# Optimization experiments

Measured on AMD Instinct MI355X. Metric: run time of the kernel, lower is better.

The kernel has to match this reference:

```python
import jax, jax.numpy as jnp
import numpy as np

B, L, H, NH, DH = 2, 4096, 768, 12, 64
W_ = 128          # one-sided sliding window
NL = 2            # encoder layers
VOCAB, OUT, FF = 50265, 384, 3072
EPS = 1e-5


def _ln(x, s, b):
    m = jnp.mean(x, axis=-1, keepdims=True)
    v = jnp.mean((x - m) ** 2, axis=-1, keepdims=True)
    return (x - m) / jnp.sqrt(v + EPS) * s + b


def _attn(x, amask, Wq, bq, Wk, bk, Wv, bv, Wo, bo):
    # x: [B,L,H]; sliding-window attention (one-sided W_) + global token 0
    def heads(Wt, bt):
        return (x @ Wt + bt).reshape(B, L, NH, DH).transpose(0, 2, 1, 3)  # [B,NH,L,DH]
    q, k, v = heads(Wq, bq), heads(Wk, bk), heads(Wv, bv)
    scale = 1.0 / np.sqrt(DH).astype(np.float32)
    C = W_
    nC = L // C
    qc = q.reshape(B, NH, nC, C, DH)

    def blocks(t):  # gather [prev, self, next] key chunks -> [B,NH,nC,3C,DH]
        tc = t.reshape(B, NH, nC, C, DH)
        tp = jnp.pad(tc, ((0, 0), (0, 0), (1, 1), (0, 0), (0, 0)))
        return jnp.concatenate([tp[:, :, :-2], tp[:, :, 1:-1], tp[:, :, 2:]], axis=3)

    k3, v3 = blocks(k), blocks(v)
    s_loc = jnp.einsum('bhncd,bhnkd->bhnck', qc, k3) * scale  # [B,NH,nC,C,3C]

    pos_k = (jnp.arange(nC)[:, None] - 1) * C + jnp.arange(3 * C)[None, :]  # [nC,3C]
    pos_q = jnp.arange(nC)[:, None] * C + jnp.arange(C)[None, :]            # [nC,C]
    within = jnp.abs(pos_q[:, :, None] - pos_k[:, None, :]) <= W_           # [nC,C,3C]
    valid = (pos_k >= 0) & (pos_k < L) & (pos_k != 0)  # key 0 handled as global column
    mk = amask[:, jnp.clip(pos_k, 0, L - 1)] > 0        # [B,nC,3C]
    m = within[None, None] & valid[None, None, :, None, :] & mk[:, None, :, None, :]
    s_loc = jnp.where(m, s_loc, -1e9)

    # every token also attends to the global token 0
    s_g = jnp.einsum('bhld,bhd->bhl', q, k[:, :, 0]) * scale  # [B,NH,L]
    s = jnp.concatenate([s_loc.reshape(B, NH, L, 3 * C), s_g[..., None]], axis=-1)
    p = jax.nn.softmax(s, axis=-1)
    p_loc = p[..., :3 * C].reshape(B, NH, nC, C, 3 * C)
    out = jnp.einsum('bhnck,bhnkd->bhncd', p_loc, v3).reshape(B, NH, L, DH)
    out = out + p[..., -1:] * v[:, :, 0][:, :, None, :]

    # global token 0 attends to everything
    s0 = jnp.einsum('bhd,bhld->bhl', q[:, :, 0], k) * scale
    s0 = jnp.where(amask[:, None, :] > 0, s0, -1e9)
    o0 = jnp.einsum('bhl,bhld->bhd', jax.nn.softmax(s0, axis=-1), v)
    out = out.at[:, :, 0, :].set(o0)

    out = out.transpose(0, 2, 1, 3).reshape(B, L, H)
    return out @ Wo + bo


def setup_inputs() -> dict:
    key = jax.random.key(0)
    ks = jax.random.split(key, 16)
    p = lambda k_, sh: 0.02 * jax.random.normal(k_, sh, jnp.float32)
    return {
        'input_ids': jax.random.randint(ks[0], (B, L), 0, VOCAB, dtype=jnp.int32),
        'attention_mask': jnp.ones((B, L), jnp.int32),
        'word_emb': p(ks[1], (VOCAB, H)),
        'pos_emb': p(ks[2], (L, H)),
        'emb_ln_s': jnp.ones((H,), jnp.float32), 'emb_ln_b': jnp.zeros((H,), jnp.float32),
        'Wq': p(ks[3], (NL, H, H)), 'bq': jnp.zeros((NL, H), jnp.float32),
        'Wk': p(ks[4], (NL, H, H)), 'bk': jnp.zeros((NL, H), jnp.float32),
        'Wv': p(ks[5], (NL, H, H)), 'bv': jnp.zeros((NL, H), jnp.float32),
        'Wo': p(ks[6], (NL, H, H)), 'bo': jnp.zeros((NL, H), jnp.float32),
        'ln1_s': jnp.ones((NL, H), jnp.float32), 'ln1_b': jnp.zeros((NL, H), jnp.float32),
        'W1': p(ks[7], (NL, H, FF)), 'b1': jnp.zeros((NL, FF), jnp.float32),
        'W2': p(ks[8], (NL, FF, H)), 'b2': jnp.zeros((NL, H), jnp.float32),
        'ln2_s': jnp.ones((NL, H), jnp.float32), 'ln2_b': jnp.zeros((NL, H), jnp.float32),
        'Wfc': p(ks[9], (H, OUT)), 'bfc': jnp.zeros((OUT,), jnp.float32),
    }


def reference(input_ids, attention_mask, word_emb, pos_emb, emb_ln_s, emb_ln_b,
              Wq, bq, Wk, bk, Wv, bv, Wo, bo, ln1_s, ln1_b,
              W1, b1, W2, b2, ln2_s, ln2_b, Wfc, bfc):
    x = word_emb[input_ids] + pos_emb[None]
    x = _ln(x, emb_ln_s, emb_ln_b)
    for l in range(NL):
        a = _attn(x, attention_mask, Wq[l], bq[l], Wk[l], bk[l], Wv[l], bv[l], Wo[l], bo[l])
        x = _ln(x + a, ln1_s[l], ln1_b[l])
        h = jax.nn.gelu(x @ W1[l] + b1[l])
        x = _ln(x + h @ W2[l] + b2[l], ln2_s[l], ln2_b[l])
    v_dn = x @ Wfc + bfc           # [B,L,OUT]
    cls = v_dn[:, 0]               # fc(last_hidden[:,0]) == v_dn[:,0]
    return v_dn, cls
```

## Files before the change

### kernel.cpp

```cpp
#include <hip/hip_runtime.h>
#include <hip/hip_bf16.h>
#include <stdint.h>

#define L_SEQ 4096
#define H_DIM 768
#define N_HEADS 12
#define D_HEAD 64
#define N_CHUNK 32
#define CHUNK 128
#define FF_DIM 3072
#define OUT_DIM 384
#define BATCH 2
#define EPS_LN 1e-5f
#define M_ROWS (BATCH * L_SEQ)
#define QKV_LD (3 * H_DIM)
#define NSEG 16

typedef unsigned short u16;
typedef __bf16 bx8 __attribute__((ext_vector_type(8)));
typedef float fx4 __attribute__((ext_vector_type(4)));
typedef u16 ux8 __attribute__((ext_vector_type(8)));

__device__ __forceinline__ u16 f2bf(float f) {
  union { float f; unsigned u; } x; x.f = f;
  unsigned r = x.u + 0x7fffu + ((x.u >> 16) & 1u);
  return (u16)(r >> 16);
}
__device__ __forceinline__ float bf2f(u16 v) {
  union { unsigned u; float f; } x; x.u = ((unsigned)v) << 16;
  return x.f;
}

__device__ __forceinline__ void gload16(const void* g, void* l) {
  __builtin_amdgcn_global_load_lds((const __attribute__((address_space(1))) void*)g,
                                   (__attribute__((address_space(3))) void*)l, 16, 0, 0);
}

template<int OUT_BF16, int DO_GELU, int DO_CLS>
__global__ __launch_bounds__(256, 3)
void gemm_s(const u16* __restrict__ A, const u16* __restrict__ Bt,
            const float* __restrict__ bias,
            float* __restrict__ Cf, u16* __restrict__ Cb,
            float* __restrict__ cls,
            int N, int K)
{
  __shared__ __align__(16) u16 As[128 * 64];
  __shared__ __align__(16) u16 Bs[128 * 64];
  const int tid = threadIdx.x;
  const int lane = tid & 63, w = tid >> 6;
  const int c16 = lane & 15, g = lane >> 4;
  const int wr = w >> 1, wc = w & 1;

  const int nbn = N >> 7;
  int id = blockIdx.x;
  id = (id & 7) * (gridDim.x >> 3) + (id >> 3);
  const int bm = id / nbn, bn = id % nbn;

  const int srow = w * 8 + (lane >> 3);
  const int schunk = (lane & 7) ^ (lane >> 3);
  const u16* sA = A + (size_t)(bm * 128 + srow) * K + schunk * 8;
  const u16* sB = Bt + (size_t)(bn * 128 + srow) * K + schunk * 8;
  const int wdst = w * 512;

  fx4 acc[4][4] = {};

  for (int k0 = 0; k0 < K; k0 += 64) {
    #pragma unroll
    for (int i = 0; i < 4; i++) {
      gload16(sA + (size_t)(i * 32) * K + k0, &As[i * 2048 + wdst]);
      gload16(sB + (size_t)(i * 32) * K + k0, &Bs[i * 2048 + wdst]);
    }
    __syncthreads();
    #pragma unroll
    for (int h = 0; h < 2; h++) {
      bx8 af[4], bf[4];
      #pragma unroll
      for (int m = 0; m < 4; m++) {
        const int row = wr * 64 + m * 16 + c16;
        af[m] = *(const bx8*)&As[row * 64 + (((h << 2) + g) ^ (c16 & 7)) * 8];
      }
      #pragma unroll
      for (int n = 0; n < 4; n++) {
        const int row = wc * 64 + n * 16 + c16;
        bf[n] = *(const bx8*)&Bs[row * 64 + (((h << 2) + g) ^ (c16 & 7)) * 8];
      }
      #pragma unroll
      for (int m = 0; m < 4; m++)
        #pragma unroll
        for (int n = 0; n < 4; n++)
          acc[m][n] = __builtin_amdgcn_mfma_f32_16x16x32_bf16(af[m], bf[n], acc[m][n], 0, 0, 0);
    }
    __syncthreads();
  }

  const int row0 = bm * 128 + wr * 64 + g * 4;
  const int col0 = bn * 128 + wc * 64 + c16;
  #pragma unroll
  for (int n = 0; n < 4; n++) {
    const int col = col0 + n * 16;
    const float bb = bias[col];
    #pragma unroll
    for (int m = 0; m < 4; m++) {
      #pragma unroll
      for (int r = 0; r < 4; r++) {
        float y = acc[m][n][r] + bb;
        if (DO_GELU) {
          const float tt = y;
          y = 0.5f * tt * (1.0f + tanhf(0.7978845608f * (tt + 0.044715f * tt * tt * tt)));
        }
        const int row = row0 + m * 16 + r;
        const size_t idx = (size_t)row * N + col;
        if (OUT_BF16) Cb[idx] = f2bf(y);
        else Cf[idx] = y;
        if (DO_CLS) {
          if ((row & (L_SEQ - 1)) == 0)
            cls[(row >> 12) * OUT_DIM + col] = y;
        }
      }
    }
  }
}

#define KV_W 384
#define P_STR 128

__global__ __launch_bounds__(512, 4)
void attn_local_kernel(const u16* __restrict__ qkv, const int* __restrict__ amask,
                       u16* __restrict__ attnout)
{
  __shared__ __align__(16) u16 Vlds[64 * KV_W];
  __shared__ __align__(16) u16 Plds[8 * 16 * P_STR];

  const int tid = threadIdx.x;
  const int lane = tid & 63, w = tid >> 6;
  const int c16 = lane & 15, g = lane >> 4;

  const int bh = blockIdx.x >> 5;
  const int n = blockIdx.x & 31;
  const int b = bh / N_HEADS, h = bh % N_HEADS;

  const u16* qkvb = qkv + (size_t)b * L_SEQ * QKV_LD + h * D_HEAD;
  const int chunk_lo = n * CHUNK - CHUNK;

  {
    const int d = lane;
    #pragma unroll
    for (int it = 0; it < 6; it++) {
      const int kb = it * 8 + w;
      ux8 vals;
      #pragma unroll
      for (int j = 0; j < 8; j++) {
        int pos = chunk_lo + kb * 8 + j;
        if (pos < 0) pos = 0;
        if (pos >= L_SEQ) pos = L_SEQ - 1;
        vals[j] = qkvb[(size_t)pos * QKV_LD + 2 * H_DIM + d];
      }
      *(ux8*)&Vlds[d * KV_W + ((kb ^ (d & 7)) << 3)] = vals;
    }
  }

  const int qrow = n * CHUNK + w * 16 + c16;
  const u16* qp = qkvb + (size_t)qrow * QKV_LD + g * 8;
  const bx8 aq0 = *(const bx8*)qp;
  const bx8 aq1 = *(const bx8*)(qp + 32);

  unsigned kvm = 0;
  #pragma unroll
  for (int kf = 0; kf < 24; kf++) {
    const int pos = chunk_lo + kf * 16 + c16;
    bool ok = (pos >= 1) && (pos < L_SEQ);
    if (ok) ok = (amask[b * L_SEQ + pos] > 0);
    kvm |= ((unsigned)ok) << kf;
  }

  fx4 s[25];
  #pragma unroll
  for (int kf = 0; kf < 25; kf++) {
    int pos = (kf == 24) ? 0 : chunk_lo + kf * 16 + c16;
    if (pos < 0 || pos >= L_SEQ) pos = 0;
    const u16* kp = qkvb + (size_t)pos * QKV_LD + H_DIM + g * 8;
    const bx8 b0 = *(const bx8*)kp;
    const bx8 b1 = *(const bx8*)(kp + 32);
    fx4 a = {};
    a = __builtin_amdgcn_mfma_f32_16x16x32_bf16(aq0, b0, a, 0, 0, 0);
    a = __builtin_amdgcn_mfma_f32_16x16x32_bf16(aq1, b1, a, 0, 0, 0);
    s[kf] = a;
  }

  const int cq = w * 16 + g * 4;
  float mx[4], sm[4];
  #pragma unroll
  for (int r = 0; r < 4; r++) mx[r] = -3.0e38f;
  #pragma unroll
  for (int kf = 0; kf < 25; kf++) {
    const int j = kf * 16 + c16;
    const bool kv = (kf < 24) ? (((kvm >> kf) & 1u) != 0) : (c16 == 0);
    #pragma unroll
    for (int r = 0; r < 4; r++) {
      const int c = cq + r;
      const bool keep = kv && (kf == 24 || (j >= c && j <= c + 256));
      const float val = keep ? s[kf][r] * 0.125f : -1.0e9f;
      s[kf][r] = val;
      mx[r] = fmaxf(mx[r], val);
    }
  }
  #pragma unroll
  for (int r = 0; r < 4; r++) {
    float m = mx[r];
    m = fmaxf(m, __shfl_xor(m, 1));
    m = fmaxf(m, __shfl_xor(m, 2));
    m = fmaxf(m, __shfl_xor(m, 4));
    m = fmaxf(m, __shfl_xor(m, 8));
    mx[r] = m;
    sm[r] = 0.f;
  }
  #pragma unroll
  for (int kf = 0; kf < 25; kf++)
    #pragma unroll
    for (int r = 0; r < 4; r++) {
      const float p = __expf(s[kf][r] - mx[r]);
      s[kf][r] = p;
      sm[r] += p;
    }
  float rinv[4];
  #pragma unroll
  for (int r = 0; r < 4; r++) {
    float t = sm[r];
    t += __shfl_xor(t, 1);
    t += __shfl_xor(t, 2);
    t += __shfl_xor(t, 4);
    t += __shfl_xor(t, 8);
    rinv[r] = 1.0f / t;
  }

  float pg[4];
  #pragma unroll
  for (int r = 0; r < 4; r++) pg[r] = __shfl(s[24][r], g * 16);

  __syncthreads();

  fx4 o[4] = {};
  u16* pb = Plds + w * 16 * P_STR;
  const int prow = (w * 16 + c16) * P_STR;
  #pragma unroll
  for (int pass = 0; pass < 4; pass++) {
    #pragma unroll
    for (int kf6 = 0; kf6 < 6; kf6++) {
      const int kf = pass * 6 + kf6;
      #pragma unroll
      for (int r = 0; r < 4; r++) {
        const int rr = g * 4 + r;
        const int jj = kf6 * 16 + c16;
        pb[rr * P_STR + (((jj >> 3) ^ (rr & 7)) << 3) + (jj & 7)] = f2bf(s[kf][r]);
      }
    }
    #pragma unroll
    for (int t = 0; t < 3; t++) {
      const int ckp = t * 4 + g;
      const bx8 pa = *(const bx8*)&Plds[prow + ((ckp ^ (c16 & 7)) << 3)];
      const int ckv = pass * 12 + ckp;
      #pragma unroll
      for (int df = 0; df < 4; df++) {
        const int vrow = df * 16 + c16;
        const bx8 vvf = *(const bx8*)&Vlds[vrow * KV_W + ((ckv ^ (c16 & 7)) << 3)];
        o[df] = __builtin_amdgcn_mfma_f32_16x16x32_bf16(pa, vvf, o[df], 0, 0, 0);
      }
    }
  }

  u16* ob = attnout + (size_t)b * L_SEQ * H_DIM + h * D_HEAD;
  const int posq = n * CHUNK + w * 16 + g * 4;
  #pragma unroll
  for (int df = 0; df < 4; df++) {
    const float v0f = bf2f(qkvb[2 * H_DIM + df * 16 + c16]);
    #pragma unroll
    for (int r = 0; r < 4; r++)
      ob[(size_t)(posq + r) * H_DIM + df * 16 + c16] =
          f2bf((o[df][r] + pg[r] * v0f) * rinv[r]);
  }
}

__global__ __launch_bounds__(256)
void attn_g_score(const u16* __restrict__ qkv, const int* __restrict__ amask,
                  float* __restrict__ sbuf, float* __restrict__ pmax)
{
  __shared__ float qs[D_HEAD];
  __shared__ float red[4];
  const int seg = blockIdx.x, bh = blockIdx.y;
  const int b = bh / N_HEADS, h = bh % N_HEADS;
  const u16* base = qkv + (size_t)b * L_SEQ * QKV_LD + h * D_HEAD;
  const int tid = threadIdx.x;

  if (tid < D_HEAD) qs[tid] = bf2f(base[tid]);
  __syncthreads();

  const int l = seg * 256 + tid;
  const ux8* kp = (const ux8*)(base + (size_t)l * QKV_LD + H_DIM);
  float dot = 0.f;
  #pragma unroll
  for (int i = 0; i < 8; i++) {
    const ux8 kv = kp[i];
    #pragma unroll
    for (int j = 0; j < 8; j++) dot += qs[i * 8 + j] * bf2f(kv[j]);
  }
  float sv = dot * 0.125f;
  if (amask[b * L_SEQ + l] == 0) sv = -1.0e9f;
  sbuf[(size_t)bh * L_SEQ + l] = sv;

  float m = sv;
  #pragma unroll
  for (int off = 32; off > 0; off >>= 1) m = fmaxf(m, __shfl_xor(m, off));
  if ((tid & 63) == 0) red[tid >> 6] = m;
  __syncthreads();
  if (tid == 0)
    pmax[bh * NSEG + seg] = fmaxf(fmaxf(red[0], red[1]), fmaxf(red[2], red[3]));
}

__global__ __launch_bounds__(256)
void attn_g_pv(const u16* __restrict__ qkv, const float* __restrict__ sbuf,
               const float* __restrict__ pmax, float* __restrict__ psum,
               float* __restrict__ po)
{
  __shared__ float es[256];
  __shared__ float red[4];
  const int seg = blockIdx.x, bh = blockIdx.y;
  const int b = bh / N_HEADS, h = bh % N_HEADS;
  const int tid = threadIdx.x;

  float M = -3.0e38f;
  #pragma unroll
  for (int i = 0; i < NSEG; i++) M = fmaxf(M, pmax[bh * NSEG + i]);

  const int l = seg * 256 + tid;
  const float e = __expf(sbuf[(size_t)bh * L_SEQ + l] - M);
  es[tid] = e;

  float t = e;
  #pragma unroll
  for (int off = 32; off > 0; off >>= 1) t += __shfl_xor(t, off);
  if ((tid & 63) == 0) red[tid >> 6] = t;
  __syncthreads();
  if (tid == 0) psum[bh * NSEG + seg] = red[0] + red[1] + red[2] + red[3];

  const int d = tid & 63, grp = tid >> 6;
  const u16* vb = qkv + (size_t)b * L_SEQ * QKV_LD + h * D_HEAD + 2 * H_DIM + d;
  float acc = 0.f;
  #pragma unroll 4
  for (int i = 0; i < 64; i++) {
    const int ll = seg * 256 + grp * 64 + i;
    acc += es[grp * 64 + i] * bf2f(vb[(size_t)ll * QKV_LD]);
  }
  po[(((size_t)bh * NSEG + seg) * 4 + grp) * D_HEAD + d] = acc;
}

__global__ __launch_bounds__(64)
void attn_g_combine(const float* __restrict__ psum, const float* __restrict__ po,
                    u16* __restrict__ attnout)
{
  const int bh = blockIdx.x;
  const int b = bh / N_HEADS, h = bh % N_HEADS;
  const int d = threadIdx.x;
  float S = 0.f;
  #pragma unroll
  for (int i = 0; i < NSEG; i++) S += psum[bh * NSEG + i];
  float acc = 0.f;
  #pragma unroll
  for (int i = 0; i < NSEG * 4; i++)
    acc += po[((size_t)bh * NSEG * 4 + i) * D_HEAD + d];
  attnout[(size_t)b * L_SEQ * H_DIM + h * D_HEAD + d] = f2bf(acc / S);
}

__device__ __forceinline__ void block_stats(float sum, float sq, float* red,
                                            float& mean, float& rstd)
{
  const int lane = threadIdx.x & 63, wv = threadIdx.x >> 6;
  #pragma unroll
  for (int off = 32; off > 0; off >>= 1) {
    sum += __shfl_xor(sum, off);
    sq  += __shfl_xor(sq, off);
  }
  if (lane == 0) { red[wv] = sum; red[4 + wv] = sq; }
  __syncthreads();
  sum = red[0] + red[1] + red[2] + red[3];
  sq  = red[4] + red[5] + red[6] + red[7];
  mean = sum * (1.0f / H_DIM);
  const float var = sq * (1.0f / H_DIM) - mean * mean;
  rstd = rsqrtf(var + EPS_LN);
}

__global__ __launch_bounds__(256)
void embed_ln_kernel(const int* __restrict__ ids, const float* __restrict__ wemb,
                     const float* __restrict__ pemb, const float* __restrict__ gam,
                     const float* __restrict__ bet, u16* __restrict__ xb)
{
  __shared__ float red[8];
  const int row = blockIdx.x, tid = threadIdx.x;
  const int l = row & (L_SEQ - 1);
  const int id = ids[row];
  float v[3]; float sum = 0.f, sq = 0.f;
  #pragma unroll
  for (int i = 0; i < 3; i++) {
    const int c = tid + i * 256;
    const float t = wemb[(size_t)id * H_DIM + c] + pemb[(size_t)l * H_DIM + c];
    v[i] = t; sum += t; sq += t * t;
  }
  float mean, rstd;
  block_stats(sum, sq, red, mean, rstd);
  #pragma unroll
  for (int i = 0; i < 3; i++) {
    const int c = tid + i * 256;
    const float y = (v[i] - mean) * rstd * gam[c] + bet[c];
    xb[(size_t)row * H_DIM + c] = f2bf(y);
  }
}

__global__ __launch_bounds__(256)
void add_ln_kernel(u16* xio, const u16* __restrict__ yin,
                   const float* __restrict__ gam, const float* __restrict__ bet)
{
  __shared__ float red[8];
  const int row = blockIdx.x, tid = threadIdx.x;
  float v[3]; float sum = 0.f, sq = 0.f;
  #pragma unroll
  for (int i = 0; i < 3; i++) {
    const int c = tid + i * 256;
    const float t = bf2f(xio[(size_t)row * H_DIM + c]) + bf2f(yin[(size_t)row * H_DIM + c]);
    v[i] = t; sum += t; sq += t * t;
  }
  float mean, rstd;
  block_stats(sum, sq, red, mean, rstd);
  #pragma unroll
  for (int i = 0; i < 3; i++) {
    const int c = tid + i * 256;
    const float y = (v[i] - mean) * rstd * gam[c] + bet[c];
    xio[(size_t)row * H_DIM + c] = f2bf(y);
  }
}

__global__ __launch_bounds__(256)
void prep_weights(const float* __restrict__ Wq, const float* __restrict__ Wk,
                  const float* __restrict__ Wv, const float* __restrict__ Wo,
                  const float* __restrict__ W1, const float* __restrict__ W2,
                  const float* __restrict__ Wfc,
                  const float* __restrict__ bq, const float* __restrict__ bk,
                  const float* __restrict__ bv,
                  u16* __restrict__ wqkvT, u16* __restrict__ woT,
                  u16* __restrict__ w1T, u16* __restrict__ w2T,
                  u16* __restrict__ wfcT, float* __restrict__ bqkv)
{
  const int t = blockIdx.x;
  const int tid = threadIdx.x;
  if (t >= 14112) {
    const int idx = t - 14112;
    const int l = idx / 9, j = idx % 9;
    const int i = j * 256 + tid;
    if (i < H_DIM)          bqkv[l * QKV_LD + i] = bq[l * H_DIM + i];
    else if (i < 2 * H_DIM) bqkv[l * QKV_LD + i] = bk[l * H_DIM + i - H_DIM];
    else if (i < 3 * H_DIM) bqkv[l * QKV_LD + i] = bv[l * H_DIM + i - 2 * H_DIM];
    return;
  }
  const float* src; u16* dst; int K, N, r;
  if (t < 13824) {
    const int l = t / 6912; r = t % 6912;
    if (r < 2304) {
      const int m = r / 576; r = r % 576; K = H_DIM; N = H_DIM;
      if (m == 0)      src = Wq + (size_t)l * H_DIM * H_DIM;
      else if (m == 1) src = Wk + (size_t)l * H_DIM * H_DIM;
      else if (m == 2) src = Wv + (size_t)l * H_DIM * H_DIM;
      else             src = Wo + (size_t)l * H_DIM * H_DIM;
      dst = (m < 3) ? wqkvT + (size_t)l * QKV_LD * H_DIM + (size_t)m * H_DIM * H_DIM
                    : woT + (size_t)l * H_DIM * H_DIM;
    } else if (r < 4608) {
      r -= 2304; K = H_DIM; N = FF_DIM;
      src = W1 + (size_t)l * H_DIM * FF_DIM;
      dst = w1T + (size_t)l * FF_DIM * H_DIM;
    } else {
      r -= 4608; K = FF_DIM; N = H_DIM;
      src = W2 + (size_t)l * FF_DIM * H_DIM;
      dst = w2T + (size_t)l * H_DIM * FF_DIM;
    }
  } else {
    r = t - 13824; K = H_DIM; N = OUT_DIM; src = Wfc; dst = wfcT;
  }
  const int ntn = N >> 5;
  const int k0 = (r / ntn) * 32, n0 = (r % ntn) * 32;
  __shared__ float tile[32][33];
  const int tx = tid & 31, ty = tid >> 5;
  #pragma unroll
  for (int i = 0; i < 32; i += 8)
    tile[ty + i][tx] = src[(size_t)(k0 + ty + i) * N + n0 + tx];
  __syncthreads();
  #pragma unroll
  for (int i = 0; i < 32; i += 8)
    dst[(size_t)(n0 + ty + i) * K + k0 + tx] = f2bf(tile[tx][ty + i]);
}

extern "C" void kernel_launch(void* const* d_in, const int* in_sizes, int n_in,
                              void* d_out, int out_size, void* d_ws, size_t ws_size,
                              hipStream_t stream)
{
  (void)in_sizes; (void)n_in; (void)out_size; (void)ws_size;
  const int*   ids   = (const int*)d_in[0];
  const int*   amask = (const int*)d_in[1];
  const float* wemb  = (const float*)d_in[2];
  const float* pemb  = (const float*)d_in[3];
  const float* elns  = (const float*)d_in[4];
  const float* elnb  = (const float*)d_in[5];
  const float* Wq    = (const float*)d_in[6];
  const float* bq    = (const float*)d_in[7];
  const float* Wk    = (const float*)d_in[8];
  const float* bk    = (const float*)d_in[9];
  const float* Wv    = (const float*)d_in[10];
  const float* bv    = (const float*)d_in[11];
  const float* Wo    = (const float*)d_in[12];
  const float* bo    = (const float*)d_in[13];
  const float* ln1s  = (const float*)d_in[14];
  const float* ln1b  = (const float*)d_in[15];
  const float* W1    = (const float*)d_in[16];
  const float* b1    = (const float*)d_in[17];
  const float* W2    = (const float*)d_in[18];
  const float* b2    = (const float*)d_in[19];
  const float* ln2s  = (const float*)d_in[20];
  const float* ln2b  = (const float*)d_in[21];
  const float* Wfc   = (const float*)d_in[22];
  const float* bfc   = (const float*)d_in[23];

  char* ws = (char*)d_ws;
  size_t off = 0;
  auto alloc = [&](size_t bytes) -> void* {
    void* p = ws + off;
    off += (bytes + 255) & ~(size_t)255;
    return p;
  };
  u16* xb     = (u16*)alloc((size_t)M_ROWS * H_DIM * 2);
  u16* projb  = (u16*)alloc((size_t)M_ROWS * H_DIM * 2);
  u16* big    = (u16*)alloc((size_t)M_ROWS * FF_DIM * 2);
  u16* attno  = (u16*)alloc((size_t)M_ROWS * H_DIM * 2);
  u16* wqkvT  = (u16*)alloc((size_t)2 * QKV_LD * H_DIM * 2);
  u16* woT    = (u16*)alloc((size_t)2 * H_DIM * H_DIM * 2);
  u16* w1T    = (u16*)alloc((size_t)2 * FF_DIM * H_DIM * 2);
  u16* w2T    = (u16*)alloc((size_t)2 * H_DIM * FF_DIM * 2);
  u16* wfcT   = (u16*)alloc((size_t)OUT_DIM * H_DIM * 2);
  float* bqkv = (float*)alloc(2 * QKV_LD * 4);
  float* gsc  = (float*)alloc((size_t)BATCH * N_HEADS * L_SEQ * 4);
  float* gpm  = (float*)alloc((size_t)BATCH * N_HEADS * NSEG * 4);
  float* gps  = (float*)alloc((size_t)BATCH * N_HEADS * NSEG * 4);
  float* gpo  = (float*)alloc((size_t)BATCH * N_HEADS * NSEG * 4 * D_HEAD * 4);

  u16* qkvb = big;
  u16* ff1  = big;

  prep_weights<<<14130, 256, 0, stream>>>(Wq, Wk, Wv, Wo, W1, W2, Wfc,
                                          bq, bk, bv,
                                          wqkvT, woT, w1T, w2T, wfcT, bqkv);
  embed_ln_kernel<<<M_ROWS, 256, 0, stream>>>(ids, wemb, pemb, elns, elnb, xb);

  for (int l = 0; l < 2; l++) {
    gemm_s<1, 0, 0><<<(M_ROWS / 128) * (QKV_LD / 128), 256, 0, stream>>>(
        xb, wqkvT + (size_t)l * QKV_LD * H_DIM, bqkv + l * QKV_LD,
        nullptr, qkvb, nullptr, QKV_LD, H_DIM);
    attn_local_kernel<<<BATCH * N_HEADS * N_CHUNK, 512, 0, stream>>>(qkvb, amask, attno);
    attn_g_score<<<dim3(NSEG, BATCH * N_HEADS), 256, 0, stream>>>(qkvb, amask, gsc, gpm);
    attn_g_pv<<<dim3(NSEG, BATCH * N_HEADS), 256, 0, stream>>>(qkvb, gsc, gpm, gps, gpo);
    attn_g_combine<<<BATCH * N_HEADS, 64, 0, stream>>>(gps, gpo, attno);
    gemm_s<1, 0, 0><<<(M_ROWS / 128) * (H_DIM / 128), 256, 0, stream>>>(
        attno, woT + (size_t)l * H_DIM * H_DIM, bo + l * H_DIM,
        nullptr, projb, nullptr, H_DIM, H_DIM);
    add_ln_kernel<<<M_ROWS, 256, 0, stream>>>(xb, projb, ln1s + l * H_DIM, ln1b + l * H_DIM);
    gemm_s<1, 1, 0><<<(M_ROWS / 128) * (FF_DIM / 128), 256, 0, stream>>>(
        xb, w1T + (size_t)l * FF_DIM * H_DIM, b1 + l * FF_DIM,
        nullptr, ff1, nullptr, FF_DIM, H_DIM);
    gemm_s<1, 0, 0><<<(M_ROWS / 128) * (H_DIM / 128), 256, 0, stream>>>(
        ff1, w2T + (size_t)l * H_DIM * FF_DIM, b2 + l * H_DIM,
        nullptr, projb, nullptr, H_DIM, FF_DIM);
    add_ln_kernel<<<M_ROWS, 256, 0, stream>>>(xb, projb, ln2s + l * H_DIM, ln2b + l * H_DIM);
  }

  float* vdn = (float*)d_out;
  float* cls = vdn + (size_t)BATCH * L_SEQ * OUT_DIM;
  gemm_s<0, 0, 1><<<(M_ROWS / 128) * (OUT_DIM / 128), 256, 0, stream>>>(
      xb, wfcT, bfc, vdn, nullptr, cls, OUT_DIM, H_DIM);
}
```

Before: 646.5 us.

## Use online softmax over key passes in local attention to cut register use

```diff
diff --git a/kernel.cpp b/kernel.cpp
--- a/kernel.cpp
+++ b/kernel.cpp
@@ -173,85 +173,114 @@
     kvm |= ((unsigned)ok) << kf;
   }
 
-  fx4 s[25];
-  #pragma unroll
-  for (int kf = 0; kf < 25; kf++) {
-    int pos = (kf == 24) ? 0 : chunk_lo + kf * 16 + c16;
-    if (pos < 0 || pos >= L_SEQ) pos = 0;
-    const u16* kp = qkvb + (size_t)pos * QKV_LD + H_DIM + g * 8;
+  const int cq = w * 16 + g * 4;
+
+  float m[4], l[4], pgv[4];
+  {
+    const u16* kp = qkvb + H_DIM + g * 8;
     const bx8 b0 = *(const bx8*)kp;
     const bx8 b1 = *(const bx8*)(kp + 32);
-    fx4 a = {};
-    a = __builtin_amdgcn_mfma_f32_16x16x32_bf16(aq0, b0, a, 0, 0, 0);
-    a = __builtin_amdgcn_mfma_f32_16x16x32_bf16(aq1, b1, a, 0, 0, 0);
-    s[kf] = a;
-  }
-
-  const int cq = w * 16 + g * 4;
-  float mx[4], sm[4];
-  #pragma unroll
-  for (int r = 0; r < 4; r++) mx[r] = -3.0e38f;
-  #pragma unroll
-  for (int kf = 0; kf < 25; kf++) {
-    const int j = kf * 16 + c16;
-    const bool kv = (kf < 24) ? (((kvm >> kf) & 1u) != 0) : (c16 == 0);
+    fx4 sg = {};
+    sg = __builtin_amdgcn_mfma_f32_16x16x32_bf16(aq0, b0, sg, 0, 0, 0);
+    sg = __builtin_amdgcn_mfma_f32_16x16x32_bf16(aq1, b1, sg, 0, 0, 0);
     #pragma unroll
     for (int r = 0; r < 4; r++) {
-      const int c = cq + r;
-      const bool keep = kv && (kf == 24 || (j >= c && j <= c + 256));
-      const float val = keep ? s[kf][r] * 0.125f : -1.0e9f;
-      s[kf][r] = val;
-      mx[r] = fmaxf(mx[r], val);
-    }
-  }
-  #pragma unroll
-  for (int r = 0; r < 4; r++) {
-    float m = mx[r];
-    m = fmaxf(m, __shfl_xor(m, 1));
-    m = fmaxf(m, __shfl_xor(m, 2));
-    m = fmaxf(m, __shfl_xor(m, 4));
-    m = fmaxf(m, __shfl_xor(m, 8));
-    mx[r] = m;
-    sm[r] = 0.f;
-  }
-  #pragma unroll
-  for (int kf = 0; kf < 25; kf++)
-    #pragma unroll
-    for (int r = 0; r < 4; r++) {
-      const float p = __expf(s[kf][r] - mx[r]);
-      s[kf][r] = p;
-      sm[r] += p;
-    }
-  float rinv[4];
-  #pragma unroll
-  for (int r = 0; r < 4; r++) {
-    float t = sm[r];
-    t += __shfl_xor(t, 1);
-    t += __shfl_xor(t, 2);
-    t += __shfl_xor(t, 4);
-    t += __shfl_xor(t, 8);
-    rinv[r] = 1.0f / t;
-  }
-
-  float pg[4];
-  #pragma unroll
-  for (int r = 0; r < 4; r++) pg[r] = __shfl(s[24][r], g * 16);
+      const float val = (c16 == 0) ? sg[r] * 0.125f : -1.0e9f;
+      float mm = val;
+      mm = fmaxf(mm, __shfl_xor(mm, 1));
+      mm = fmaxf(mm, __shfl_xor(mm, 2));
+      mm = fmaxf(mm, __shfl_xor(mm, 4));
+      mm = fmaxf(mm, __shfl_xor(mm, 8));
+      m[r] = mm;
+      pgv[r] = __expf(val - mm);
+      float t = pgv[r];
+      t += __shfl_xor(t, 1);
+      t += __shfl_xor(t, 2);
+      t += __shfl_xor(t, 4);
+      t += __shfl_xor(t, 8);
+      l[r] = t;
+    }
+  }
 
   __syncthreads();
 
   fx4 o[4] = {};
   u16* pb = Plds + w * 16 * P_STR;
   const int prow = (w * 16 + c16) * P_STR;
+
   #pragma unroll
   for (int pass = 0; pass < 4; pass++) {
+    fx4 s[6];
     #pragma unroll
     for (int kf6 = 0; kf6 < 6; kf6++) {
       const int kf = pass * 6 + kf6;
+      int pos = chunk_lo + kf * 16 + c16;
+      if (pos < 0 || pos >= L_SEQ) pos = 0;
+      const u16* kp = qkvb + (size_t)pos * QKV_LD + H_DIM + g * 8;
+      const bx8 b0 = *(const bx8*)kp;
+      const bx8 b1 = *(const bx8*)(kp + 32);
+      fx4 a = {};
+      a = __builtin_amdgcn_mfma_f32_16x16x32_bf16(aq0, b0, a, 0, 0, 0);
+      a = __builtin_amdgcn_mfma_f32_16x16x32_bf16(aq1, b1, a, 0, 0, 0);
+      s[kf6] = a;
+    }
+    float pmax[4];
+    #pragma unroll
+    for (int r = 0; r < 4; r++) pmax[r] = -3.0e38f;
+    #pragma unroll
+    for (int kf6 = 0; kf6 < 6; kf6++) {
+      const int kf = pass * 6 + kf6;
+      const int j = kf * 16 + c16;
+      const bool kv = ((kvm >> kf) & 1u) != 0;
+      #pragma unroll
+      for (int r = 0; r < 4; r++) {
+        const int c = cq + r;
+        const bool keep = kv && (j >= c && j <= c + 256);
+        const float val = keep ? s[kf6][r] * 0.125f : -1.0e9f;
+        s[kf6][r] = val;
+        pmax[r] = fmaxf(pmax[r], val);
+      }
+    }
+    #pragma unroll
+    for (int r = 0; r < 4; r++) {
+      float mm = pmax[r];
+      mm = fmaxf(mm, __shfl_xor(mm, 1));
+      mm = fmaxf(mm, __shfl_xor(mm, 2));
+      mm = fmaxf(mm, __shfl_xor(mm, 4));
+      mm = fmaxf(mm, __shfl_xor(mm, 8));
+      const float newm = fmaxf(m[r], mm);
+      const float scale = __expf(m[r] - newm);
+      m[r] = newm;
+      l[r] *= scale;
+      pgv[r] *= scale;
+      #pragma unroll
+      for (int df = 0; df < 4; df++) o[df][r] *= scale;
+    }
+    float lsum[4] = {0.f, 0.f, 0.f, 0.f};
+    #pragma unroll
+    for (int kf6 = 0; kf6 < 6; kf6++)
+      #pragma unroll
+      for (int r = 0; r < 4; r++) {
+        const float p = __expf(s[kf6][r] - m[r]);
+        s[kf6][r] = p;
+        lsum[r] += p;
+      }
+    #pragma unroll
+    for (int r = 0; r < 4; r++) {
+      float t = lsum[r];
+      t += __shfl_xor(t, 1);
+      t += __shfl_xor(t, 2);
+      t += __shfl_xor(t, 4);
+      t += __shfl_xor(t, 8);
+      l[r] += t;
+    }
+    #pragma unroll
+    for (int kf6 = 0; kf6 < 6; kf6++) {
       #pragma unroll
       for (int r = 0; r < 4; r++) {
         const int rr = g * 4 + r;
         const int jj = kf6 * 16 + c16;
-        pb[rr * P_STR + (((jj >> 3) ^ (rr & 7)) << 3) + (jj & 7)] = f2bf(s[kf][r]);
+        pb[rr * P_STR + (((jj >> 3) ^ (rr & 7)) << 3) + (jj & 7)] = f2bf(s[kf6][r]);
       }
     }
     #pragma unroll
@@ -268,6 +297,12 @@
     }
   }
 
+  float rinv[4], pg[4];
+  #pragma unroll
+  for (int r = 0; r < 4; r++) {
+    rinv[r] = 1.0f / l[r];
+    pg[r] = __shfl(pgv[r], g * 16);
+  }
   u16* ob = attnout + (size_t)b * L_SEQ * H_DIM + h * D_HEAD;
   const int posq = n * CHUNK + w * 16 + g * 4;
   #pragma unroll
```

Result: faster. 629.8 us (-2.6%).
